# Kernel tuning notes

Measured on AMD Instinct MI355X. Metric: run time of the kernel, lower is better.

## Reference

```python
import jax, jax.numpy as jnp
import numpy as np

B, T, A_DIM, Z_DIM, K = 128, 80, 32, 64, 16


def setup_inputs() -> dict:
    key = jax.random.key(0)
    k1, k2, k3, k4 = jax.random.split(key, 4)
    obs = jax.random.normal(k1, (B, T, A_DIM), jnp.float32)
    alpha_logits = jax.random.normal(k2, (B, T, K), jnp.float32)
    # torch init: A = eye(z) repeated K times; small noise keeps 80-step recursion stable
    A_K = jnp.eye(Z_DIM, dtype=jnp.float32)[None] + 0.005 * jax.random.normal(k3, (K, Z_DIM, Z_DIM), jnp.float32)
    # torch init: C = 0.05 * randn
    C_K = 0.05 * jax.random.normal(k4, (K, A_DIM, Z_DIM), jnp.float32)
    return {"obs": obs, "alpha_logits": alpha_logits, "A_K": A_K, "C_K": C_K}


def _kalman(obs, A, C):
    # obs [B,T,a], A [B,T,z,z], C [B,T,a,z]
    Bq, Tq, a_dim = obs.shape
    z_dim = A.shape[-1]
    dt = obs.dtype
    Q = 0.08 * jnp.eye(z_dim, dtype=dt)
    R = 0.03 * jnp.eye(a_dim, dtype=dt)
    I = jnp.eye(z_dim, dtype=dt)

    obs_t = jnp.swapaxes(obs, 0, 1)          # [T,B,a]
    A_t = jnp.swapaxes(A, 0, 1)              # [T,B,z,z]
    C_t = jnp.swapaxes(C, 0, 1)              # [T,B,a,z]
    A_next = jnp.concatenate([A_t[1:], A_t[-1:]], axis=0)  # A[t+1]; last unused

    mu0 = jnp.zeros((Bq, z_dim), dt)
    sig0 = jnp.broadcast_to(20.0 * I, (Bq, z_dim, z_dim))

    def filt_step(carry, inp):
        mu_p, sig_p, mu_prev = carry
        At, Anx, Ct, y = inp
        CtT = jnp.swapaxes(Ct, -1, -2)
        S = Ct @ sig_p @ CtT + R                       # [B,a,a]
        Kg = sig_p @ CtT @ jnp.linalg.inv(S)            # [B,z,a]
        Amu = jnp.einsum('bij,bj->bi', At, mu_prev)     # A_t mu_{t-1}
        err = y - jnp.einsum('bij,bj->bi', Ct, Amu)
        mu_f = Amu + jnp.einsum('bij,bj->bi', Kg, err)
        sig_f = (I - Kg @ Ct) @ sig_p
        mu_pn = jnp.einsum('bij,bj->bi', Anx, mu_f)     # prediction with A_{t+1}
        sig_pn = Anx @ sig_f @ jnp.swapaxes(Anx, -1, -2) + Q
        return (mu_pn, sig_pn, mu_f), (mu_f, sig_f, mu_p, sig_p)

    _, (mu_f, sig_f, mu_p, sig_p) = jax.lax.scan(
        filt_step, (mu0, sig0, mu0), (A_t, A_next, C_t, obs_t))

    def smooth_step(carry, inp):
        mu_s, sig_s = carry
        mf, sf, Anx, mpn, spn = inp
        J = sf @ jnp.swapaxes(Anx, -1, -2) @ jnp.linalg.inv(spn)
        mu = mf + jnp.einsum('bij,bj->bi', J, mu_s - mpn)
        sig = sf + J @ (sig_s - spn) @ jnp.swapaxes(J, -1, -2)
        return (mu, sig), (mu, sig)

    init = (mu_f[-1], sig_f[-1])
    _, (mu_sm, sig_sm) = jax.lax.scan(
        smooth_step, init,
        (mu_f[:-1], sig_f[:-1], A_t[1:], mu_p[1:], sig_p[1:]),
        reverse=True)
    mu_sm = jnp.concatenate([mu_sm, mu_f[-1:]], axis=0)
    sig_sm = jnp.concatenate([sig_sm, sig_f[-1:]], axis=0)
    return jnp.swapaxes(mu_sm, 0, 1), jnp.swapaxes(sig_sm, 0, 1)  # [B,T,z], [B,T,z,z]


def reference(obs, alpha_logits, A_K, C_K):
    w = jax.nn.softmax(alpha_logits, axis=-1)                # [B,T,K]
    A = jnp.einsum('btk,kij->btij', w, A_K)                  # [B,T,z,z]
    C = jnp.einsum('btk,kij->btij', w, C_K)                  # [B,T,a,z]
    return _kalman(obs, A, C)
```

## Files before the change

### kernel.cpp

```cpp
#include <hip/hip_runtime.h>

#define B_ 128
#define T_ 80
#define AD 32
#define ZD 64
#define KD 16
#define S8 68
#define SC 36

__device__ __forceinline__ float4 ld4(const float* p) { return *(const float4*)p; }
__device__ __forceinline__ void st4f(float* p, float4 v) { *(float4*)p = v; }

__device__ __forceinline__ float4 comb4(float4 c, float4 x0, float4 x1, float4 x2, float4 x3) {
    return make_float4(c.x*x0.x + c.y*x1.x + c.z*x2.x + c.w*x3.x,
                       c.x*x0.y + c.y*x1.y + c.z*x2.y + c.w*x3.y,
                       c.x*x0.z + c.y*x1.z + c.z*x2.z + c.w*x3.z,
                       c.x*x0.w + c.y*x1.w + c.z*x2.w + c.w*x3.w);
}

__device__ __forceinline__ void pinv4(float4 q0, float4 q1, float4 q2, float4 q3,
                                      float4& pi0, float4& pi1, float4& pi2, float4& pi3)
{
    const float ra = 1.0f / (q0.x*q1.y - q0.y*q1.x);
    const float ai00 =  q1.y*ra, ai01 = -q0.y*ra, ai10 = -q1.x*ra, ai11 = q0.x*ra;
    const float ca00 = q2.x*ai00 + q2.y*ai10, ca01 = q2.x*ai01 + q2.y*ai11;
    const float ca10 = q3.x*ai00 + q3.y*ai10, ca11 = q3.x*ai01 + q3.y*ai11;
    const float s00 = q2.z - (ca00*q0.z + ca01*q1.z), s01 = q2.w - (ca00*q0.w + ca01*q1.w);
    const float s10 = q3.z - (ca10*q0.z + ca11*q1.z), s11 = q3.w - (ca10*q0.w + ca11*q1.w);
    const float rs = 1.0f / (s00*s11 - s01*s10);
    const float si00 = s11*rs, si01 = -s01*rs, si10 = -s10*rs, si11 = s00*rs;
    const float ab00 = ai00*q0.z + ai01*q1.z, ab01 = ai00*q0.w + ai01*q1.w;
    const float ab10 = ai10*q0.z + ai11*q1.z, ab11 = ai10*q0.w + ai11*q1.w;
    const float t00 = ab00*si00 + ab01*si10, t01 = ab00*si01 + ab01*si11;
    const float t10 = ab10*si00 + ab11*si10, t11 = ab10*si01 + ab11*si11;
    const float tl00 = ai00 + (t00*ca00 + t01*ca10), tl01 = ai01 + (t00*ca01 + t01*ca11);
    const float tl10 = ai10 + (t10*ca00 + t11*ca10), tl11 = ai11 + (t10*ca01 + t11*ca11);
    const float bl00 = -(si00*ca00 + si01*ca10), bl01 = -(si00*ca01 + si01*ca11);
    const float bl10 = -(si10*ca00 + si11*ca10), bl11 = -(si10*ca01 + si11*ca11);
    pi0 = make_float4(tl00, tl01, -t00, -t01);
    pi1 = make_float4(tl10, tl11, -t10, -t11);
    pi2 = make_float4(bl00, bl01, si00, si01);
    pi3 = make_float4(bl10, bl11, si10, si11);
}

template<int KL, int AS, int BS, bool ATRANS>
__device__ __forceinline__ void mm64(const float* __restrict__ Pa, const float* __restrict__ Qb,
                                     float acc[2][4], int r2, int c4)
{
#pragma unroll 8
    for (int k = 0; k < KL; k++) {
        float aA, aB;
        if (ATRANS) { aA = Pa[k * AS + r2];   aB = Pa[k * AS + r2 + 1]; }
        else        { aA = Pa[r2 * AS + k];   aB = Pa[(r2 + 1) * AS + k]; }
        const float4 bv = ld4(&Qb[k * BS + c4]);
        acc[0][0] += aA * bv.x; acc[0][1] += aA * bv.y; acc[0][2] += aA * bv.z; acc[0][3] += aA * bv.w;
        acc[1][0] += aB * bv.x; acc[1][1] += aB * bv.y; acc[1][2] += aB * bv.z; acc[1][3] += aB * bv.w;
    }
}

__global__ __launch_bounds__(512, 2)
void kvae_kernel(const float* __restrict__ obs, const float* __restrict__ logits,
                 const float* __restrict__ AK, const float* __restrict__ CK,
                 float* __restrict__ out)
{
    __shared__ __align__(16) float W[T_ * KD];
    __shared__ __align__(16) float Am[ZD * S8];
    __shared__ __align__(16) float At[ZD * S8];
    __shared__ __align__(16) float SP[ZD * S8];
    __shared__ __align__(16) float SF[ZD * S8];
    __shared__ __align__(16) float Mm[ZD * S8];
    __shared__ __align__(16) float Pool[9984];
    __shared__ __align__(16) float pvL[512];
    __shared__ __align__(16) float pvR[512];
    __shared__ __align__(16) float fbb[512];
    __shared__ __align__(16) float pvE[8];
    __shared__ __align__(16) float y_s[32];
    __shared__ __align__(16) float errv[32];
    __shared__ __align__(16) float uev[32];
    __shared__ __align__(16) float mup[64];
    __shared__ __align__(16) float muf[64];
    __shared__ __align__(16) float mus[64];
    __shared__ __align__(16) float mpn[64];
    __shared__ __align__(16) float dv[64];

    float* T1 = Pool;
    float* CM = Pool + 2176;
    float* CT = Pool + 4352;
    float* U_ = Pool + 6656;
    float* S_ = Pool + 8832;
    float* Xb = Pool;
    float* SG = Pool + 4352;

    const int tid = threadIdx.x;
    const int b   = blockIdx.x;

    const int r16 = tid >> 4;
    const int cg  = tid & 15;
    const int c4  = cg << 2;
    const int c2  = cg << 1;
    const int r2  = r16 << 1;
    const int gi  = tid >> 3;
    const int gs  = tid & 7;

    const float* obs_b = obs    + (size_t)b * T_ * AD;
    const float* lg_b  = logits + (size_t)b * T_ * KD;
    float* omu = out + (size_t)b * T_ * ZD;
    float* osg = out + (size_t)B_ * T_ * ZD + (size_t)b * T_ * ZD * ZD;
    const float4* AK4 = (const float4*)AK;
    const float4* CK4 = (const float4*)CK;

    auto mixA = [&](int tt) {
#pragma unroll
        for (int rr = 0; rr < 2; rr++) {
            const int r = r2 + rr;
            float4 a = make_float4(0.f, 0.f, 0.f, 0.f);
#pragma unroll
            for (int k = 0; k < KD; k++) {
                const float wk = W[tt * KD + k];
                const float4 v = AK4[k * 1024 + r * 16 + cg];
                a.x += wk * v.x; a.y += wk * v.y; a.z += wk * v.z; a.w += wk * v.w;
            }
            st4f(&Am[r * S8 + c4], a);
            At[(c4 + 0) * S8 + r] = a.x; At[(c4 + 1) * S8 + r] = a.y;
            At[(c4 + 2) * S8 + r] = a.z; At[(c4 + 3) * S8 + r] = a.w;
        }
    };
    auto mixC = [&](int tt) {
        float4 a = make_float4(0.f, 0.f, 0.f, 0.f);
#pragma unroll
        for (int k = 0; k < KD; k++) {
            const float wk = W[tt * KD + k];
            const float4 v = CK4[k * 512 + r16 * 16 + cg];
            a.x += wk * v.x; a.y += wk * v.y; a.z += wk * v.z; a.w += wk * v.w;
        }
        st4f(&CM[r16 * S8 + c4], a);
        CT[(c4 + 0) * SC + r16] = a.x; CT[(c4 + 1) * SC + r16] = a.y;
        CT[(c4 + 2) * SC + r16] = a.z; CT[(c4 + 3) * SC + r16] = a.w;
    };

    if (tid < T_) {
        float l[KD]; float mx = -1e30f;
#pragma unroll
        for (int k = 0; k < KD; k++) { l[k] = lg_b[tid * KD + k]; mx = fmaxf(mx, l[k]); }
        float s = 0.f;
#pragma unroll
        for (int k = 0; k < KD; k++) { l[k] = expf(l[k] - mx); s += l[k]; }
        const float inv = 1.0f / s;
#pragma unroll
        for (int k = 0; k < KD; k++) W[tid * KD + k] = l[k] * inv;
    }
#pragma unroll
    for (int rr = 0; rr < 2; rr++) {
        const int r = r2 + rr;
#pragma unroll
        for (int j = 0; j < 4; j++) SP[r * S8 + c4 + j] = (r == c4 + j) ? 20.0f : 0.0f;
    }
    if (tid < ZD) mup[tid] = 0.0f;
    __syncthreads();

    for (int t = 0; t < T_; t++) {
        if (t < T_ - 1) mixA(t + 1);
        mixC(t);
        if (tid < AD) y_s[tid] = obs_b[t * AD + tid];
        __syncthreads();

        {
            float a0 = 0, a1 = 0, a2 = 0, a3 = 0;
            const float* pa = CM + r16 * S8;
#pragma unroll 8
            for (int k = 0; k < ZD; k++) {
                const float a = pa[k];
                const float4 bv = ld4(&SP[k * S8 + c4]);
                a0 += a * bv.x; a1 += a * bv.y; a2 += a * bv.z; a3 += a * bv.w;
            }
            T1[r16 * S8 + c4 + 0] = a0; T1[r16 * S8 + c4 + 1] = a1;
            T1[r16 * S8 + c4 + 2] = a2; T1[r16 * S8 + c4 + 3] = a3;
        }
        __syncthreads();

        {
            float a0 = 0, a1 = 0;
            const float* pa = T1 + r16 * S8;
#pragma unroll 8
            for (int k = 0; k < ZD; k++) {
                const float a = pa[k];
                const float2 bv = *(const float2*)&CT[k * SC + c2];
                a0 += a * bv.x; a1 += a * bv.y;
            }
            if (r16 == c2)     a0 += 0.03f;
            if (r16 == c2 + 1) a1 += 0.03f;
            S_[r16 * SC + c2] = a0; S_[r16 * SC + c2 + 1] = a1;
        }
        if (tid < AD) {
            float s = 0.f;
#pragma unroll
            for (int k4 = 0; k4 < ZD; k4 += 4) {
                const float4 cm = ld4(&CM[tid * S8 + k4]);
                const float4 mu = ld4(&mup[k4]);
                s += cm.x*mu.x + cm.y*mu.y + cm.z*mu.z + cm.w*mu.w;
            }
            errv[tid] = y_s[tid] - s;
        }
        __syncthreads();

        {
            const int hi = r16, hs = cg;
            float4 aL = make_float4(0, 0, 0, 0);
            float4 aR = ld4(&T1[hi * S8 + hs * 4]);
            float e = 0.f;
            if (hs < 8) aL = ld4(&S_[hi * SC + hs * 4]);
            if (hs == 15) e = errv[hi];
            if (hi < 4) {
                if (hs < 8) st4f(&pvL[hi * 32 + hs * 4], aL);
                st4f(&pvR[hi * 64 + hs * 4], aR);
                if (hs == 15) pvE[hi] = e;
            }
            if (hs == 0) st4f(&fbb[hi * 4], aL);
            __syncthreads();

#pragma unroll 2
            for (int j = 0; j < 8; ++j) {
                const int par = j & 1, nb = par ^ 1;
                const bool isp = (hi >> 2) == j;
                const float4 f  = ld4(&fbb[par * 128 + hi * 4]);
                const float4 q0 = ld4(&fbb[par * 128 + (4 * j + 0) * 4]);
                const float4 q1 = ld4(&fbb[par * 128 + (4 * j + 1) * 4]);
                const float4 q2 = ld4(&fbb[par * 128 + (4 * j + 2) * 4]);
                const float4 q3 = ld4(&fbb[par * 128 + (4 * j + 3) * 4]);
                float4 pi0, pi1, pi2, pi3;
                pinv4(q0, q1, q2, q3, pi0, pi1, pi2, pi3);
                const int rr = hi & 3;
                const float4 coef = isp ? (rr == 0 ? pi0 : rr == 1 ? pi1 : rr == 2 ? pi2 : pi3)
                                        : comb4(f, pi0, pi1, pi2, pi3);
                {
                    const float4 x0 = ld4(&pvR[par * 256 + 0 * 64 + hs * 4]);
                    const float4 x1 = ld4(&pvR[par * 256 + 1 * 64 + hs * 4]);
                    const float4 x2 = ld4(&pvR[par * 256 + 2 * 64 + hs * 4]);
                    const float4 x3 = ld4(&pvR[par * 256 + 3 * 64 + hs * 4]);
                    const float4 c = comb4(coef, x0, x1, x2, x3);
                    if (isp) aR = c;
                    else { aR.x -= c.x; aR.y -= c.y; aR.z -= c.z; aR.w -= c.w; }
                }
                if (hs < 8) {
                    const float4 x0 = ld4(&pvL[par * 128 + 0 * 32 + hs * 4]);
                    const float4 x1 = ld4(&pvL[par * 128 + 1 * 32 + hs * 4]);
                    const float4 x2 = ld4(&pvL[par * 128 + 2 * 32 + hs * 4]);
                    const float4 x3 = ld4(&pvL[par * 128 + 3 * 32 + hs * 4]);
                    const float4 c = comb4(coef, x0, x1, x2, x3);
                    if (isp) aL = c;
                    else { aL.x -= c.x; aL.y -= c.y; aL.z -= c.z; aL.w -= c.w; }
                }
                if (hs == 15) {
                    const float e0 = pvE[par * 4 + 0], e1 = pvE[par * 4 + 1];
                    const float e2 = pvE[par * 4 + 2], e3 = pvE[par * 4 + 3];
                    const float ce = coef.x * e0 + coef.y * e1 + coef.z * e2 + coef.w * e3;
                    if (isp) e = ce; else e -= ce;
                }
                if (j < 7) {
                    if ((hi >> 2) == j + 1) {
                        if (hs < 8) st4f(&pvL[nb * 128 + (hi & 3) * 32 + hs * 4], aL);
                        st4f(&pvR[nb * 256 + (hi & 3) * 64 + hs * 4], aR);
                        if (hs == 15) pvE[nb * 4 + (hi & 3)] = e;
                    }
                    if (hs == j + 1) st4f(&fbb[nb * 128 + hi * 4], aL);
                }
                __syncthreads();
            }
            st4f(&U_[hi * S8 + hs * 4], aR);
            if (hs == 15) uev[hi] = e;
        }
        __syncthreads();

        {
            float acc[2][4] = {};
            mm64<AD, S8, S8, true>(T1, U_, acc, r2, c4);
            float* og = osg + (size_t)t * ZD * ZD;
#pragma unroll
            for (int rr = 0; rr < 2; rr++) {
                const int r = r2 + rr;
                const float4 sp = ld4(&SP[r * S8 + c4]);
                const float4 v = make_float4(sp.x - acc[rr][0], sp.y - acc[rr][1],
                                             sp.z - acc[rr][2], sp.w - acc[rr][3]);
                st4f(&SF[r * S8 + c4], v);
                *(float4*)(og + r * ZD + c4) = v;
            }
        }
        if (tid < ZD) {
            float s = 0.f;
#pragma unroll
            for (int k = 0; k < AD; k++) s += T1[k * S8 + tid] * uev[k];
            const float v = mup[tid] + s;
            muf[tid] = v;
            omu[t * ZD + tid] = v;
        }
        __syncthreads();

        if (t < T_ - 1) {
            {
                float acc[2][4] = {};
                mm64<ZD, S8, S8, false>(Am, SF, acc, r2, c4);
#pragma unroll
                for (int rr = 0; rr < 2; rr++)
                    st4f(&Mm[(r2 + rr) * S8 + c4],
                         make_float4(acc[rr][0], acc[rr][1], acc[rr][2], acc[rr][3]));
            }
            __syncthreads();
            {
                float acc[2][4] = {};
                mm64<ZD, S8, S8, false>(Mm, At, acc, r2, c4);
#pragma unroll
                for (int rr = 0; rr < 2; rr++) {
                    const int r = r2 + rr;
#pragma unroll
                    for (int j = 0; j < 4; j++)
                        SP[r * S8 + c4 + j] = acc[rr][j] + ((r == c4 + j) ? 0.08f : 0.0f);
                }
            }
            if (tid >= 448) {
                const int i = tid - 448;
                float s = 0.f;
                const float* pa = Am + i * S8;
#pragma unroll 8
                for (int k = 0; k < ZD; k++) s += pa[k] * muf[k];
                mup[i] = s;
            }
            __syncthreads();
        }
    }

#pragma unroll
    for (int rr = 0; rr < 2; rr++)
        st4f(&SG[(r2 + rr) * S8 + c4], ld4(&SF[(r2 + rr) * S8 + c4]));
    if (tid < ZD) mus[tid] = muf[tid];
    __syncthreads();

    for (int t = T_ - 2; t >= 0; t--) {
        mixA(t + 1);
        {
            const float4* og4 = (const float4*)(osg + (size_t)t * ZD * ZD);
#pragma unroll
            for (int rr = 0; rr < 2; rr++)
                st4f(&SF[(r2 + rr) * S8 + c4], og4[(r2 + rr) * 16 + cg]);
        }
        if (tid >= 448) muf[tid - 448] = omu[t * ZD + (tid - 448)];
        __syncthreads();

        {
            float acc[2][4] = {};
            mm64<ZD, S8, S8, false>(Am, SF, acc, r2, c4);
#pragma unroll
            for (int rr = 0; rr < 2; rr++)
                st4f(&Mm[(r2 + rr) * S8 + c4],
                     make_float4(acc[rr][0], acc[rr][1], acc[rr][2], acc[rr][3]));
        }
        if (tid >= 448) {
            const int i = tid - 448;
            float s = 0.f;
            const float* pa = Am + i * S8;
#pragma unroll 8
            for (int k = 0; k < ZD; k++) s += pa[k] * muf[k];
            mpn[i] = s;
        }
        __syncthreads();

        {
            float acc[2][4] = {};
            mm64<ZD, S8, S8, false>(Mm, At, acc, r2, c4);
#pragma unroll
            for (int rr = 0; rr < 2; rr++) {
                const int r = r2 + rr;
#pragma unroll
                for (int j = 0; j < 4; j++)
                    SP[r * S8 + c4 + j] = acc[rr][j] + ((r == c4 + j) ? 0.08f : 0.0f);
            }
        }
        if (tid >= 448) { const int i = tid - 448; dv[i] = mus[i] - mpn[i]; }
        __syncthreads();

        {
            float4 aL0 = ld4(&SP[gi * S8 + gs * 8]);
            float4 aL1 = ld4(&SP[gi * S8 + gs * 8 + 4]);
            float4 aR0 = ld4(&Mm[gi * S8 + gs * 8]);
            float4 aR1 = ld4(&Mm[gi * S8 + gs * 8 + 4]);
            if (gi < 4) {
                st4f(&pvL[gi * 64 + gs * 8], aL0); st4f(&pvL[gi * 64 + gs * 8 + 4], aL1);
                st4f(&pvR[gi * 64 + gs * 8], aR0); st4f(&pvR[gi * 64 + gs * 8 + 4], aR1);
            }
            if (gs == 0) st4f(&fbb[gi * 4], aL0);
            __syncthreads();

#pragma unroll 2
            for (int j = 0; j < 16; ++j) {
                const int par = j & 1, nb = par ^ 1;
                const bool isp = (gi >> 2) == j;
                const float4 f  = ld4(&fbb[par * 256 + gi * 4]);
                const float4 q0 = ld4(&fbb[par * 256 + (4 * j + 0) * 4]);
                const float4 q1 = ld4(&fbb[par * 256 + (4 * j + 1) * 4]);
                const float4 q2 = ld4(&fbb[par * 256 + (4 * j + 2) * 4]);
                const float4 q3 = ld4(&fbb[par * 256 + (4 * j + 3) * 4]);
                float4 pi0, pi1, pi2, pi3;
                pinv4(q0, q1, q2, q3, pi0, pi1, pi2, pi3);
                const int rr = gi & 3;
                const float4 coef = isp ? (rr == 0 ? pi0 : rr == 1 ? pi1 : rr == 2 ? pi2 : pi3)
                                        : comb4(f, pi0, pi1, pi2, pi3);
                {
                    const float4 x0 = ld4(&pvL[par * 256 + 0 * 64 + gs * 8]);
                    const float4 x1 = ld4(&pvL[par * 256 + 1 * 64 + gs * 8]);
                    const float4 x2 = ld4(&pvL[par * 256 + 2 * 64 + gs * 8]);
                    const float4 x3 = ld4(&pvL[par * 256 + 3 * 64 + gs * 8]);
                    const float4 c = comb4(coef, x0, x1, x2, x3);
                    if (isp) aL0 = c;
                    else { aL0.x -= c.x; aL0.y -= c.y; aL0.z -= c.z; aL0.w -= c.w; }
                }
                {
                    const float4 x0 = ld4(&pvL[par * 256 + 0 * 64 + gs * 8 + 4]);
                    const float4 x1 = ld4(&pvL[par * 256 + 1 * 64 + gs * 8 + 4]);
                    const float4 x2 = ld4(&pvL[par * 256 + 2 * 64 + gs * 8 + 4]);
                    const float4 x3 = ld4(&pvL[par * 256 + 3 * 64 + gs * 8 + 4]);
                    const float4 c = comb4(coef, x0, x1, x2, x3);
                    if (isp) aL1 = c;
                    else { aL1.x -= c.x; aL1.y -= c.y; aL1.z -= c.z; aL1.w -= c.w; }
                }
                {
                    const float4 x0 = ld4(&pvR[par * 256 + 0 * 64 + gs * 8]);
                    const float4 x1 = ld4(&pvR[par * 256 + 1 * 64 + gs * 8]);
                    const float4 x2 = ld4(&pvR[par * 256 + 2 * 64 + gs * 8]);
                    const float4 x3 = ld4(&pvR[par * 256 + 3 * 64 + gs * 8]);
                    const float4 c = comb4(coef, x0, x1, x2, x3);
                    if (isp) aR0 = c;
                    else { aR0.x -= c.x; aR0.y -= c.y; aR0.z -= c.z; aR0.w -= c.w; }
                }
                {
                    const float4 x0 = ld4(&pvR[par * 256 + 0 * 64 + gs * 8 + 4]);
                    const float4 x1 = ld4(&pvR[par * 256 + 1 * 64 + gs * 8 + 4]);
                    const float4 x2 = ld4(&pvR[par * 256 + 2 * 64 + gs * 8 + 4]);
                    const float4 x3 = ld4(&pvR[par * 256 + 3 * 64 + gs * 8 + 4]);
                    const float4 c = comb4(coef, x0, x1, x2, x3);
                    if (isp) aR1 = c;
                    else { aR1.x -= c.x; aR1.y -= c.y; aR1.z -= c.z; aR1.w -= c.w; }
                }
                if (j < 15) {
                    if ((gi >> 2) == j + 1) {
                        const int rn = gi & 3;
                        st4f(&pvL[nb * 256 + rn * 64 + gs * 8], aL0);
                        st4f(&pvL[nb * 256 + rn * 64 + gs * 8 + 4], aL1);
                        st4f(&pvR[nb * 256 + rn * 64 + gs * 8], aR0);
                        st4f(&pvR[nb * 256 + rn * 64 + gs * 8 + 4], aR1);
                    }
                    if (gs == ((j + 1) >> 1))
                        st4f(&fbb[nb * 256 + gi * 4], ((j + 1) & 1) ? aL1 : aL0);
                }
                __syncthreads();
            }
            st4f(&Xb[gi * S8 + gs * 8], aR0);
            st4f(&Xb[gi * S8 + gs * 8 + 4], aR1);
        }
        __syncthreads();

        {
            float acc[2][4] = {};
            mm64<ZD, S8, S8, false>(SG, Xb, acc, r2, c4);
#pragma unroll
            for (int rr = 0; rr < 2; rr++) {
                const int r = r2 + rr;
                const float4 m = ld4(&Mm[r * S8 + c4]);
                SP[r * S8 + c4 + 0] = acc[rr][0] - m.x;
                SP[r * S8 + c4 + 1] = acc[rr][1] - m.y;
                SP[r * S8 + c4 + 2] = acc[rr][2] - m.z;
                SP[r * S8 + c4 + 3] = acc[rr][3] - m.w;
            }
        }
        __syncthreads();

        {
            float acc[2][4] = {};
            mm64<ZD, S8, S8, true>(Xb, SP, acc, r2, c4);
            float* og = osg + (size_t)t * ZD * ZD;
#pragma unroll
            for (int rr = 0; rr < 2; rr++) {
                const int r = r2 + rr;
                const float4 sf = ld4(&SF[r * S8 + c4]);
                const float4 v = make_float4(sf.x + acc[rr][0], sf.y + acc[rr][1],
                                             sf.z + acc[rr][2], sf.w + acc[rr][3]);
                st4f(&SG[r * S8 + c4], v);
                *(float4*)(og + r * ZD + c4) = v;
            }
        }
        if (tid < ZD) {
            float s = 0.f;
#pragma unroll 8
            for (int k = 0; k < ZD; k++) s += Xb[k * S8 + tid] * dv[k];
            const float v = muf[tid] + s;
            mus[tid] = v;
            omu[t * ZD + tid] = v;
        }
        __syncthreads();
    }
}

extern "C" void kernel_launch(void* const* d_in, const int* in_sizes, int n_in,
                              void* d_out, int out_size, void* d_ws, size_t ws_size,
                              hipStream_t stream) {
    const float* obs = (const float*)d_in[0];
    const float* lg  = (const float*)d_in[1];
    const float* AK  = (const float*)d_in[2];
    const float* CK  = (const float*)d_in[3];
    (void)d_ws; (void)ws_size; (void)in_sizes; (void)n_in; (void)out_size;
    kvae_kernel<<<dim3(B_), dim3(512), 0, stream>>>(obs, lg, AK, CK, (float*)d_out);
}
```

Baseline: 3.609 ms.

## Use 8-wide pivot blocks in Gauss-Jordan solves to halve barrier steps

The blocked Gauss-Jordan eliminations for the 32x32 innovation covariance and the 64x64 smoother solve now use 8x8 pivot blocks, inverted through a Schur complement of two 4x4 inverses, instead of 4x4 blocks. This halves the number of elimination iterations and so the number of __syncthreads barriers per time step. Left-side column blocks that are already eliminated are also skipped. In exchange, every thread does more redundant pivot-inverse arithmetic, shared buffers double in size, and register pressure goes up.

```diff
diff --git a/kernel.cpp b/kernel.cpp
--- a/kernel.cpp
+++ b/kernel.cpp
@@ -11,11 +11,24 @@
 __device__ __forceinline__ float4 ld4(const float* p) { return *(const float4*)p; }
 __device__ __forceinline__ void st4f(float* p, float4 v) { *(float4*)p = v; }
 
+__device__ __forceinline__ float4 add4(float4 a, float4 b) {
+    return make_float4(a.x + b.x, a.y + b.y, a.z + b.z, a.w + b.w);
+}
+__device__ __forceinline__ float4 sub4(float4 a, float4 b) {
+    return make_float4(a.x - b.x, a.y - b.y, a.z - b.z, a.w - b.w);
+}
 __device__ __forceinline__ float4 comb4(float4 c, float4 x0, float4 x1, float4 x2, float4 x3) {
     return make_float4(c.x*x0.x + c.y*x1.x + c.z*x2.x + c.w*x3.x,
                        c.x*x0.y + c.y*x1.y + c.z*x2.y + c.w*x3.y,
                        c.x*x0.z + c.y*x1.z + c.z*x2.z + c.w*x3.z,
                        c.x*x0.w + c.y*x1.w + c.z*x2.w + c.w*x3.w);
+}
+__device__ __forceinline__ float4 comb8(float4 a, float4 b, const float* base, int off) {
+    const float4 c = comb4(a, ld4(base + off), ld4(base + 64 + off),
+                              ld4(base + 128 + off), ld4(base + 192 + off));
+    const float4 d = comb4(b, ld4(base + 256 + off), ld4(base + 320 + off),
+                              ld4(base + 384 + off), ld4(base + 448 + off));
+    return add4(c, d);
 }
 
 __device__ __forceinline__ void pinv4(float4 q0, float4 q1, float4 q2, float4 q3,
@@ -43,6 +56,35 @@
     pi3 = make_float4(bl10, bl11, si10, si11);
 }
 
+__device__ __forceinline__ void solve8(const float* qb, float4 fA, float4 fB,
+                                       float4& cA, float4& cB)
+{
+    const float4 p0 = ld4(qb + 0),  q0 = ld4(qb + 4);
+    const float4 p1 = ld4(qb + 8),  q1 = ld4(qb + 12);
+    const float4 p2 = ld4(qb + 16), q2 = ld4(qb + 20);
+    const float4 p3 = ld4(qb + 24), q3 = ld4(qb + 28);
+    const float4 r0 = ld4(qb + 32), s0 = ld4(qb + 36);
+    const float4 r1 = ld4(qb + 40), s1 = ld4(qb + 44);
+    const float4 r2 = ld4(qb + 48), s2 = ld4(qb + 52);
+    const float4 r3 = ld4(qb + 56), s3 = ld4(qb + 60);
+    float4 pi0, pi1, pi2, pi3;
+    pinv4(p0, p1, p2, p3, pi0, pi1, pi2, pi3);
+    const float4 pq0 = comb4(pi0, q0, q1, q2, q3);
+    const float4 pq1 = comb4(pi1, q0, q1, q2, q3);
+    const float4 pq2 = comb4(pi2, q0, q1, q2, q3);
+    const float4 pq3 = comb4(pi3, q0, q1, q2, q3);
+    const float4 t0 = sub4(s0, comb4(r0, pq0, pq1, pq2, pq3));
+    const float4 t1 = sub4(s1, comb4(r1, pq0, pq1, pq2, pq3));
+    const float4 t2 = sub4(s2, comb4(r2, pq0, pq1, pq2, pq3));
+    const float4 t3 = sub4(s3, comb4(r3, pq0, pq1, pq2, pq3));
+    float4 ti0, ti1, ti2, ti3;
+    pinv4(t0, t1, t2, t3, ti0, ti1, ti2, ti3);
+    const float4 w = sub4(fB, comb4(fA, pq0, pq1, pq2, pq3));
+    cB = comb4(w, ti0, ti1, ti2, ti3);
+    const float4 v = sub4(fA, comb4(cB, r0, r1, r2, r3));
+    cA = comb4(v, pi0, pi1, pi2, pi3);
+}
+
 template<int KL, int AS, int BS, bool ATRANS>
 __device__ __forceinline__ void mm64(const float* __restrict__ Pa, const float* __restrict__ Qb,
                                      float acc[2][4], int r2, int c4)
@@ -70,10 +112,10 @@
     __shared__ __align__(16) float SF[ZD * S8];
     __shared__ __align__(16) float Mm[ZD * S8];
     __shared__ __align__(16) float Pool[9984];
-    __shared__ __align__(16) float pvL[512];
-    __shared__ __align__(16) float pvR[512];
-    __shared__ __align__(16) float fbb[512];
-    __shared__ __align__(16) float pvE[8];
+    __shared__ __align__(16) float pvL[1024];
+    __shared__ __align__(16) float pvR[1024];
+    __shared__ __align__(16) float fbb[1024];
+    __shared__ __align__(16) float pvE[16];
     __shared__ __align__(16) float y_s[32];
     __shared__ __align__(16) float errv[32];
     __shared__ __align__(16) float uev[32];
@@ -210,59 +252,53 @@
             float e = 0.f;
             if (hs < 8) aL = ld4(&S_[hi * SC + hs * 4]);
             if (hs == 15) e = errv[hi];
-            if (hi < 4) {
-                if (hs < 8) st4f(&pvL[hi * 32 + hs * 4], aL);
+            if (hi < 8) {
+                if (hs < 8) st4f(&pvL[hi * 64 + hs * 4], aL);
                 st4f(&pvR[hi * 64 + hs * 4], aR);
                 if (hs == 15) pvE[hi] = e;
             }
-            if (hs == 0) st4f(&fbb[hi * 4], aL);
+            if (hs == 0) st4f(&fbb[hi * 8], aL);
+            if (hs == 1) st4f(&fbb[hi * 8 + 4], aL);
             __syncthreads();
 
 #pragma unroll 2
-            for (int j = 0; j < 8; ++j) {
+            for (int j = 0; j < 4; ++j) {
                 const int par = j & 1, nb = par ^ 1;
-                const bool isp = (hi >> 2) == j;
-                const float4 f  = ld4(&fbb[par * 128 + hi * 4]);
-                const float4 q0 = ld4(&fbb[par * 128 + (4 * j + 0) * 4]);
-                const float4 q1 = ld4(&fbb[par * 128 + (4 * j + 1) * 4]);
-                const float4 q2 = ld4(&fbb[par * 128 + (4 * j + 2) * 4]);
-                const float4 q3 = ld4(&fbb[par * 128 + (4 * j + 3) * 4]);
-                float4 pi0, pi1, pi2, pi3;
-                pinv4(q0, q1, q2, q3, pi0, pi1, pi2, pi3);
-                const int rr = hi & 3;
-                const float4 coef = isp ? (rr == 0 ? pi0 : rr == 1 ? pi1 : rr == 2 ? pi2 : pi3)
-                                        : comb4(f, pi0, pi1, pi2, pi3);
+                const bool isp = (hi >> 3) == j;
+                const int i8 = hi & 7;
+                float4 fA, fB;
+                if (isp) {
+                    fA = make_float4(i8 == 0, i8 == 1, i8 == 2, i8 == 3);
+                    fB = make_float4(i8 == 4, i8 == 5, i8 == 6, i8 == 7);
+                } else {
+                    fA = ld4(&fbb[par * 256 + hi * 8]);
+                    fB = ld4(&fbb[par * 256 + hi * 8 + 4]);
+                }
+                float4 cA, cB;
+                solve8(&fbb[par * 256 + j * 64], fA, fB, cA, cB);
                 {
-                    const float4 x0 = ld4(&pvR[par * 256 + 0 * 64 + hs * 4]);
-                    const float4 x1 = ld4(&pvR[par * 256 + 1 * 64 + hs * 4]);
-                    const float4 x2 = ld4(&pvR[par * 256 + 2 * 64 + hs * 4]);
-                    const float4 x3 = ld4(&pvR[par * 256 + 3 * 64 + hs * 4]);
-                    const float4 c = comb4(coef, x0, x1, x2, x3);
-                    if (isp) aR = c;
-                    else { aR.x -= c.x; aR.y -= c.y; aR.z -= c.z; aR.w -= c.w; }
-                }
-                if (hs < 8) {
-                    const float4 x0 = ld4(&pvL[par * 128 + 0 * 32 + hs * 4]);
-                    const float4 x1 = ld4(&pvL[par * 128 + 1 * 32 + hs * 4]);
-                    const float4 x2 = ld4(&pvL[par * 128 + 2 * 32 + hs * 4]);
-                    const float4 x3 = ld4(&pvL[par * 128 + 3 * 32 + hs * 4]);
-                    const float4 c = comb4(coef, x0, x1, x2, x3);
-                    if (isp) aL = c;
-                    else { aL.x -= c.x; aL.y -= c.y; aL.z -= c.z; aL.w -= c.w; }
+                    const float4 c = comb8(cA, cB, &pvR[par * 512], hs * 4);
+                    if (isp) aR = c; else aR = sub4(aR, c);
+                }
+                if (hs < 8 && (hs >> 1) > j - 1) {
+                    const float4 c = comb8(cA, cB, &pvL[par * 512], hs * 4);
+                    if (isp) aL = c; else aL = sub4(aL, c);
                 }
                 if (hs == 15) {
-                    const float e0 = pvE[par * 4 + 0], e1 = pvE[par * 4 + 1];
-                    const float e2 = pvE[par * 4 + 2], e3 = pvE[par * 4 + 3];
-                    const float ce = coef.x * e0 + coef.y * e1 + coef.z * e2 + coef.w * e3;
+                    const float4 e03 = ld4(&pvE[par * 8]);
+                    const float4 e47 = ld4(&pvE[par * 8 + 4]);
+                    const float ce = cA.x*e03.x + cA.y*e03.y + cA.z*e03.z + cA.w*e03.w
+                                   + cB.x*e47.x + cB.y*e47.y + cB.z*e47.z + cB.w*e47.w;
                     if (isp) e = ce; else e -= ce;
                 }
-                if (j < 7) {
-                    if ((hi >> 2) == j + 1) {
-                        if (hs < 8) st4f(&pvL[nb * 128 + (hi & 3) * 32 + hs * 4], aL);
-                        st4f(&pvR[nb * 256 + (hi & 3) * 64 + hs * 4], aR);
-                        if (hs == 15) pvE[nb * 4 + (hi & 3)] = e;
+                if (j < 3) {
+                    if ((hi >> 3) == j + 1) {
+                        st4f(&pvR[nb * 512 + i8 * 64 + hs * 4], aR);
+                        if (hs < 8 && (hs >> 1) > j) st4f(&pvL[nb * 512 + i8 * 64 + hs * 4], aL);
+                        if (hs == 15) pvE[nb * 8 + i8] = e;
                     }
-                    if (hs == j + 1) st4f(&fbb[nb * 128 + hi * 4], aL);
+                    if (hs == 2 * (j + 1))     st4f(&fbb[nb * 256 + hi * 8], aL);
+                    if (hs == 2 * (j + 1) + 1) st4f(&fbb[nb * 256 + hi * 8 + 4], aL);
                 }
                 __syncthreads();
             }
@@ -382,73 +418,53 @@
             float4 aL1 = ld4(&SP[gi * S8 + gs * 8 + 4]);
             float4 aR0 = ld4(&Mm[gi * S8 + gs * 8]);
             float4 aR1 = ld4(&Mm[gi * S8 + gs * 8 + 4]);
-            if (gi < 4) {
+            if (gi < 8) {
                 st4f(&pvL[gi * 64 + gs * 8], aL0); st4f(&pvL[gi * 64 + gs * 8 + 4], aL1);
                 st4f(&pvR[gi * 64 + gs * 8], aR0); st4f(&pvR[gi * 64 + gs * 8 + 4], aR1);
             }
-            if (gs == 0) st4f(&fbb[gi * 4], aL0);
+            if (gs == 0) { st4f(&fbb[gi * 8], aL0); st4f(&fbb[gi * 8 + 4], aL1); }
             __syncthreads();
 
 #pragma unroll 2
-            for (int j = 0; j < 16; ++j) {
+            for (int j = 0; j < 8; ++j) {
                 const int par = j & 1, nb = par ^ 1;
-                const bool isp = (gi >> 2) == j;
-                const float4 f  = ld4(&fbb[par * 256 + gi * 4]);
-                const float4 q0 = ld4(&fbb[par * 256 + (4 * j + 0) * 4]);
-                const float4 q1 = ld4(&fbb[par * 256 + (4 * j + 1) * 4]);
-                const float4 q2 = ld4(&fbb[par * 256 + (4 * j + 2) * 4]);
-                const float4 q3 = ld4(&fbb[par * 256 + (4 * j + 3) * 4]);
-                float4 pi0, pi1, pi2, pi3;
-                pinv4(q0, q1, q2, q3, pi0, pi1, pi2, pi3);
-                const int rr = gi & 3;
-                const float4 coef = isp ? (rr == 0 ? pi0 : rr == 1 ? pi1 : rr == 2 ? pi2 : pi3)
-                                        : comb4(f, pi0, pi1, pi2, pi3);
+                const bool isp = (gi >> 3) == j;
+                const int i8 = gi & 7;
+                float4 fA, fB;
+                if (isp) {
+                    fA = make_float4(i8 == 0, i8 == 1, i8 == 2, i8 == 3);
+                    fB = make_float4(i8 == 4, i8 == 5, i8 == 6, i8 == 7);
+                } else {
+                    fA = ld4(&fbb[par * 512 + gi * 8]);
+                    fB = ld4(&fbb[par * 512 + gi * 8 + 4]);
+                }
+                float4 cA, cB;
+                solve8(&fbb[par * 512 + j * 64], fA, fB, cA, cB);
                 {
-                    const float4 x0 = ld4(&pvL[par * 256 + 0 * 64 + gs * 8]);
-                    const float4 x1 = ld4(&pvL[par * 256 + 1 * 64 + gs * 8]);
-                    const float4 x2 = ld4(&pvL[par * 256 + 2 * 64 + gs * 8]);
-                    const float4 x3 = ld4(&pvL[par * 256 + 3 * 64 + gs * 8]);
-                    const float4 c = comb4(coef, x0, x1, x2, x3);
-                    if (isp) aL0 = c;
-                    else { aL0.x -= c.x; aL0.y -= c.y; aL0.z -= c.z; aL0.w -= c.w; }
-                }
-                {
-                    const float4 x0 = ld4(&pvL[par * 256 + 0 * 64 + gs * 8 + 4]);
-                    const float4 x1 = ld4(&pvL[par * 256 + 1 * 64 + gs * 8 + 4]);
-                    const float4 x2 = ld4(&pvL[par * 256 + 2 * 64 + gs * 8 + 4]);
-                    const float4 x3 = ld4(&pvL[par * 256 + 3 * 64 + gs * 8 + 4]);
-                    const float4 c = comb4(coef, x0, x1, x2, x3);
-                    if (isp) aL1 = c;
-                    else { aL1.x -= c.x; aL1.y -= c.y; aL1.z -= c.z; aL1.w -= c.w; }
-                }
-                {
-                    const float4 x0 = ld4(&pvR[par * 256 + 0 * 64 + gs * 8]);
-                    const float4 x1 = ld4(&pvR[par * 256 + 1 * 64 + gs * 8]);
-                    const float4 x2 = ld4(&pvR[par * 256 + 2 * 64 + gs * 8]);
-                    const float4 x3 = ld4(&pvR[par * 256 + 3 * 64 + gs * 8]);
-                    const float4 c = comb4(coef, x0, x1, x2, x3);
-                    if (isp) aR0 = c;
-                    else { aR0.x -= c.x; aR0.y -= c.y; aR0.z -= c.z; aR0.w -= c.w; }
-                }
-                {
-                    const float4 x0 = ld4(&pvR[par * 256 + 0 * 64 + gs * 8 + 4]);
-                    const float4 x1 = ld4(&pvR[par * 256 + 1 * 64 + gs * 8 + 4]);
-                    const float4 x2 = ld4(&pvR[par * 256 + 2 * 64 + gs * 8 + 4]);
-                    const float4 x3 = ld4(&pvR[par * 256 + 3 * 64 + gs * 8 + 4]);
-                    const float4 c = comb4(coef, x0, x1, x2, x3);
-                    if (isp) aR1 = c;
-                    else { aR1.x -= c.x; aR1.y -= c.y; aR1.z -= c.z; aR1.w -= c.w; }
-                }
-                if (j < 15) {
-                    if ((gi >> 2) == j + 1) {
-                        const int rn = gi & 3;
-                        st4f(&pvL[nb * 256 + rn * 64 + gs * 8], aL0);
-                        st4f(&pvL[nb * 256 + rn * 64 + gs * 8 + 4], aL1);
-                        st4f(&pvR[nb * 256 + rn * 64 + gs * 8], aR0);
-                        st4f(&pvR[nb * 256 + rn * 64 + gs * 8 + 4], aR1);
+                    const float4 c0 = comb8(cA, cB, &pvR[par * 512], gs * 8);
+                    const float4 c1 = comb8(cA, cB, &pvR[par * 512], gs * 8 + 4);
+                    if (isp) { aR0 = c0; aR1 = c1; }
+                    else     { aR0 = sub4(aR0, c0); aR1 = sub4(aR1, c1); }
+                }
+                if (gs > j - 1) {
+                    const float4 c0 = comb8(cA, cB, &pvL[par * 512], gs * 8);
+                    const float4 c1 = comb8(cA, cB, &pvL[par * 512], gs * 8 + 4);
+                    if (isp) { aL0 = c0; aL1 = c1; }
+                    else     { aL0 = sub4(aL0, c0); aL1 = sub4(aL1, c1); }
+                }
+                if (j < 7) {
+                    if ((gi >> 3) == j + 1) {
+                        st4f(&pvR[nb * 512 + i8 * 64 + gs * 8], aR0);
+                        st4f(&pvR[nb * 512 + i8 * 64 + gs * 8 + 4], aR1);
+                        if (gs > j) {
+                            st4f(&pvL[nb * 512 + i8 * 64 + gs * 8], aL0);
+                            st4f(&pvL[nb * 512 + i8 * 64 + gs * 8 + 4], aL1);
+                        }
                     }
-                    if (gs == ((j + 1) >> 1))
-                        st4f(&fbb[nb * 256 + gi * 4], ((j + 1) & 1) ? aL1 : aL0);
+                    if (gs == j + 1) {
+                        st4f(&fbb[nb * 512 + gi * 8], aL0);
+                        st4f(&fbb[nb * 512 + gi * 8 + 4], aL1);
+                    }
                 }
                 __syncthreads();
             }
```

After: 4.878 ms. +35.1%, slower.
